# Performance work log

Hardware: AMD Instinct MI355X
Metric: run time of the kernel (lower is better)

## Reference

```python
import jax, jax.numpy as jnp
import numpy as np

B, N, F, H, N_ITERS = 64, 256, 16, 256, 10


def setup_inputs() -> dict:
    key = jax.random.key(0)
    ks = jax.random.split(key, 20)
    s = 0.05
    jets = jax.random.normal(ks[0], (B, N, F), dtype=jnp.float32)
    # row-normalized dense adjacency (D^-1 A style)
    a = jax.random.uniform(ks[1], (B, N, N), dtype=jnp.float32)
    dads = a / jnp.sum(a, axis=-1, keepdims=True)
    p = lambda k, sh: jax.random.normal(k, sh, dtype=jnp.float32) * s
    return {
        'jets': jets, 'dads': dads,
        'W_emb': p(ks[2], (F, H)), 'b_emb': jnp.zeros((H,), jnp.float32),
        'W_msg': p(ks[3], (H, H)), 'b_msg': jnp.zeros((H,), jnp.float32),
        # GRU vertex update: input = concat(message[H], s[F]) -> H
        'Wz': p(ks[4], (H + F, H)), 'Uz': p(ks[5], (H, H)), 'bz': jnp.zeros((H,), jnp.float32),
        'Wr': p(ks[6], (H + F, H)), 'Ur': p(ks[7], (H, H)), 'br': jnp.zeros((H,), jnp.float32),
        'Wh': p(ks[8], (H + F, H)), 'Uh': p(ks[9], (H, H)), 'bh': jnp.zeros((H,), jnp.float32),
        'W_r1': p(ks[10], (H, H)), 'b_r1': jnp.zeros((H,), jnp.float32),
        'W_r2': p(ks[11], (H, H)), 'b_r2': jnp.zeros((H,), jnp.float32),
    }


def reference(jets, dads, W_emb, b_emb, W_msg, b_msg,
              Wz, Uz, bz, Wr, Ur, br, Wh, Uh, bh,
              W_r1, b_r1, W_r2, b_r2):
    # Embedding: [B,N,F] -> [B,N,H]
    h = jnp.tanh(jets @ W_emb + b_emb)
    for _ in range(N_ITERS):
        # Message: linear then adjacency aggregation + tanh
        m = jnp.tanh(jnp.matmul(dads, h @ W_msg + b_msg))  # [B,N,H]
        # GRU-style vertex update; input = concat(message, original features s)
        x = jnp.concatenate([m, jets], axis=-1)            # [B,N,H+F]
        z = jax.nn.sigmoid(x @ Wz + h @ Uz + bz)
        r = jax.nn.sigmoid(x @ Wr + h @ Ur + br)
        h_tilde = jnp.tanh(x @ Wh + (r * h) @ Uh + bh)
        h = (1.0 - z) * h + z * h_tilde
    # Readout: per-node MLP then sum over nodes -> [B,H]
    out = jnp.sum(jnp.tanh(h @ W_r1 + b_r1) @ W_r2 + b_r2, axis=1)
    return out
```

## Files before the change

kernel.cpp:

```cpp
#include <hip/hip_runtime.h>

#define DEVI __device__ __forceinline__

typedef __attribute__((ext_vector_type(4))) float f32x4;
typedef __attribute__((ext_vector_type(8))) short s16x8;
typedef unsigned short u16;
typedef unsigned int u32;

#define WST 288
#define SROW 264
#define AST 264

#define WAITVM(n) __builtin_amdgcn_s_waitcnt(((n)&0xF) | 0x70 | 0xF00 | (((n)>>4)<<14))

DEVI u16 f2bf(float x){
  u32 u = __float_as_uint(x);
  u = (u + 0x7fffu + ((u >> 16) & 1u)) >> 16;
  return (u16)u;
}
DEVI float bf2f(u16 v){ return __uint_as_float(((u32)v) << 16); }

DEVI float fsigm(float x){ return __builtin_amdgcn_rcpf(1.f + __builtin_amdgcn_exp2f(-1.442695041f * x)); }
DEVI float ftanh(float x){ float e = __builtin_amdgcn_exp2f(2.885390082f * x); return 1.f - 2.f * __builtin_amdgcn_rcpf(e + 1.f); }

DEVI s16x8 ld8(const u16* p){ return *(const s16x8*)p; }

DEVI f32x4 ld4bf(const u16* p){
  uint2 v = *(const uint2*)p;
  f32x4 r;
  r[0] = bf2f((u16)(v.x & 0xffff)); r[1] = bf2f((u16)(v.x >> 16));
  r[2] = bf2f((u16)(v.y & 0xffff)); r[3] = bf2f((u16)(v.y >> 16));
  return r;
}

DEVI void st4bf(u16* p, float a, float b, float c, float d){
  uint2 v;
  v.x = (u32)f2bf(a) | ((u32)f2bf(b) << 16);
  v.y = (u32)f2bf(c) | ((u32)f2bf(d) << 16);
  *(uint2*)p = v;
}

#define MFMA(a,b,c) __builtin_amdgcn_mfma_f32_16x16x32_bf16((a),(b),(c),0,0,0)

DEVI void dma2(const u16* lanebase, int rowStrideElems, int c, u16* ldsbase){
#pragma unroll
  for(int q = 0; q < 2; q++){
    const u16* g = lanebase + (size_t)q*16*rowStrideElems + c*32;
    __builtin_amdgcn_global_load_lds((__attribute__((address_space(1))) const void*)g,
                                     (__attribute__((address_space(3))) void*)(ldsbase + q*512),
                                     16, 0, 0);
  }
}
#define AFRAG(buf, t) ld8(&(buf)[(t)*512 + ln*32 + ((qd ^ ((ln>>1)&3))*8)])

__global__ void k_prep(
  const float* __restrict__ jets, const float* __restrict__ dads, const float* __restrict__ W_emb,
  const float* __restrict__ W_msg, const float* __restrict__ Wz, const float* __restrict__ Uz,
  const float* __restrict__ Wr, const float* __restrict__ Ur, const float* __restrict__ Wh,
  const float* __restrict__ Uh, const float* __restrict__ W_r1,
  u16* __restrict__ jp, u16* __restrict__ dadsb, u16* __restrict__ Wet, u16* __restrict__ Wmt,
  u16* __restrict__ Wzt, u16* __restrict__ Uzt, u16* __restrict__ Wrt, u16* __restrict__ Urt,
  u16* __restrict__ Wht, u16* __restrict__ Uht, u16* __restrict__ Wr1t)
{
  int blk = blockIdx.x, tid = threadIdx.x;
  if(blk < 1280){
    int mi = blk >> 8, k = blk & 255, j = tid;
    const float* src; u16* dst;
    switch(mi){
      case 0: src = W_msg; dst = Wmt;  break;
      case 1: src = Uz;    dst = Uzt;  break;
      case 2: src = Ur;    dst = Urt;  break;
      case 3: src = Uh;    dst = Uht;  break;
      default: src = W_r1; dst = Wr1t; break;
    }
    dst[j*256 + k] = f2bf(src[k*256 + j]);
  } else if(blk < 2144){
    int q = blk - 1280; int mi = q / 288; int k = q - mi*288; int j = tid;
    const float* src; u16* dst;
    switch(mi){ case 0: src = Wz; dst = Wzt; break; case 1: src = Wr; dst = Wrt; break; default: src = Wh; dst = Wht; break; }
    dst[j*WST + k] = (k < 272) ? f2bf(src[k*256 + j]) : (u16)0;
  } else if(blk < 2176){
    int idx = (blk - 2144)*256 + tid;
    int j = idx >> 5, k = idx & 31;
    Wet[idx] = (k < 16) ? f2bf(W_emb[k*256 + j]) : (u16)0;
  } else if(blk < 4224){
    int idx = (blk - 2176)*256 + tid;
    int n = idx >> 5, k = idx & 31;
    jp[idx] = (k < 16) ? f2bf(jets[n*16 + k]) : (u16)0;
  } else {
    int idx = (blk - 4224)*256 + tid;
    f32x4 v = *(const f32x4*)(dads + (size_t)idx*4);
    st4bf(dadsb + (size_t)idx*4, v[0], v[1], v[2], v[3]);
  }
}

__global__ __launch_bounds__(256,3) void k_embed(
  u16* __restrict__ h, u16* __restrict__ hmo,
  const u16* __restrict__ jp, const u16* __restrict__ Wet, const float* __restrict__ be,
  const u16* __restrict__ Wmt, const float* __restrict__ bm)
{
  __shared__ u16 hbuf[16*SROW];
  const int tid = threadIdx.x;
  const int wv = tid >> 6, lane = tid & 63, ln = lane & 15, qd = lane >> 4;
  const int n0 = blockIdx.x * 16;
  const int b  = n0 >> 8;
  const int nb = n0 & 255;
  const int nodeA = n0 + ln;

  s16x8 jfr = ld8(jp + (size_t)nodeA*32 + qd*8);
#pragma unroll
  for(int t = 0; t < 4; t++){
    int j0 = (wv*4 + t) * 16;
    f32x4 acc = {0.f,0.f,0.f,0.f};
    s16x8 a = ld8(Wet + (size_t)(j0 + ln)*32 + qd*8);
    acc = MFMA(a, jfr, acc);
    f32x4 bv = *(const f32x4*)(be + j0 + qd*4);
    f32x4 hv;
#pragma unroll
    for(int r = 0; r < 4; r++) hv[r] = ftanh(acc[r] + bv[r]);
    st4bf(h + (size_t)nodeA*256 + j0 + qd*4, hv[0], hv[1], hv[2], hv[3]);
    st4bf(&hbuf[ln*SROW + j0 + qd*4], hv[0], hv[1], hv[2], hv[3]);
  }
  __syncthreads();

  s16x8 af[8];
#pragma unroll
  for(int c = 0; c < 8; c++) af[c] = ld8(&hbuf[ln*SROW + c*32 + qd*8]);
#pragma unroll
  for(int tp = 0; tp < 2; tp++){
    int j0 = (wv*4 + tp*2) * 16, j1 = j0 + 16;
    f32x4 a0 = {0.f,0.f,0.f,0.f}, a1 = {0.f,0.f,0.f,0.f};
#pragma unroll
    for(int c = 0; c < 8; c++){
      a0 = MFMA(af[c], ld8(Wmt + (size_t)(j0 + ln)*256 + c*32 + qd*8), a0);
      a1 = MFMA(af[c], ld8(Wmt + (size_t)(j1 + ln)*256 + c*32 + qd*8), a1);
    }
    float b0 = bm[j0 + ln], b1 = bm[j1 + ln];
    st4bf(hmo + (size_t)(b*256 + j0 + ln)*256 + nb + qd*4, a0[0]+b0, a0[1]+b0, a0[2]+b0, a0[3]+b0);
    st4bf(hmo + (size_t)(b*256 + j1 + ln)*256 + nb + qd*4, a1[0]+b1, a1[1]+b1, a1[2]+b1, a1[3]+b1);
  }
}

__global__ __launch_bounds__(512,1) void k_gru(
  u16* __restrict__ h,
  const u16* __restrict__ hmi, u16* __restrict__ hmo,
  const u16* __restrict__ dadsb, const u16* __restrict__ jp,
  const u16* __restrict__ Wzt, const u16* __restrict__ Wrt, const u16* __restrict__ Wht,
  const u16* __restrict__ Uzt, const u16* __restrict__ Urt, const u16* __restrict__ Uht,
  const u16* __restrict__ Wmt,
  const float* __restrict__ bz, const float* __restrict__ br, const float* __restrict__ bhb,
  const float* __restrict__ bm)
{
  __shared__ u16 smM[64*AST];
  __shared__ u16 smB[64*AST];
  __shared__ __align__(16) u16 stg[8][2][2][1024];
  const int tid = threadIdx.x;
  const int wv = tid >> 6, lane = tid & 63, ln = lane & 15, qd = lane >> 4;
  const int blk   = blockIdx.x;
  const int batch = (blk & 7) * 8 + (blk >> 5);
  const int group = (blk >> 3) & 3;
  const int n0 = batch * 256 + group * 64;
  const int b  = batch;
  const int nb = group * 64;
  const int j0w = wv * 32;

  u16* s0 = &stg[wv][0][0][0];
  u16* s1 = &stg[wv][1][0][0];
  u16* u0 = &stg[wv][0][1][0];
  u16* u1 = &stg[wv][1][1][0];

  const int rw = lane >> 2;
  const int cs = ((lane & 3) ^ ((lane >> 3) & 3)) * 8;

  const u16* laneA = hmi + (size_t)(b*256 + j0w + rw)*256 + cs;
  dma2(laneA, 256, 0, s0);

  s16x8 jB[4];
#pragma unroll
  for(int i = 0; i < 4; i++) jB[i] = ld8(jp + (size_t)(n0 + i*16 + ln)*32 + qd*8);

  {
    f32x4 acc[2][4];
#pragma unroll
    for(int t = 0; t < 2; t++)
#pragma unroll
      for(int i = 0; i < 4; i++) acc[t][i] = (f32x4){0.f,0.f,0.f,0.f};
    s16x8 Bf[4], Bn[4];
#pragma unroll
    for(int i = 0; i < 4; i++) Bf[i] = ld8(dadsb + (size_t)(n0 + i*16 + ln)*256 + qd*8);
#pragma unroll
    for(int c = 0; c < 8; c++){
      u16* cur = (c & 1) ? s1 : s0;
      if(c < 7){
        dma2(laneA, 256, c+1, (c & 1) ? s0 : s1);
#pragma unroll
        for(int i = 0; i < 4; i++) Bn[i] = ld8(dadsb + (size_t)(n0 + i*16 + ln)*256 + (c+1)*32 + qd*8);
        WAITVM(6);
      } else {
        WAITVM(0);
      }
#pragma unroll
      for(int t = 0; t < 2; t++){
        s16x8 A = AFRAG(cur, t);
#pragma unroll
        for(int i = 0; i < 4; i++) acc[t][i] = MFMA(A, Bf[i], acc[t][i]);
      }
      if(c < 7){
#pragma unroll
        for(int i = 0; i < 4; i++) Bf[i] = Bn[i];
      }
    }
#pragma unroll
    for(int t = 0; t < 2; t++)
#pragma unroll
      for(int i = 0; i < 4; i++)
        st4bf(&smM[(i*16 + ln)*AST + j0w + t*16 + qd*4],
              ftanh(acc[t][i][0]), ftanh(acc[t][i][1]), ftanh(acc[t][i][2]), ftanh(acc[t][i][3]));
  }
  const u16* laneWr = Wrt + (size_t)(j0w + rw)*WST + cs;
  const u16* laneUr = Urt + (size_t)(j0w + rw)*256 + cs;
  dma2(laneWr, WST, 0, s0);
  dma2(laneUr, 256, 0, u0);
  __syncthreads();

  {
    f32x4 acc[2][4];
#pragma unroll
    for(int t = 0; t < 2; t++)
#pragma unroll
      for(int i = 0; i < 4; i++) acc[t][i] = (f32x4){0.f,0.f,0.f,0.f};
    s16x8 Aj[2];
#pragma unroll
    for(int t = 0; t < 2; t++) Aj[t] = ld8(Wrt + (size_t)(j0w + t*16 + ln)*WST + 256 + qd*8);
    s16x8 Bh[4], Bn[4];
#pragma unroll
    for(int i = 0; i < 4; i++) Bh[i] = ld8(h + (size_t)(n0 + i*16 + ln)*256 + qd*8);
#pragma unroll
    for(int c = 0; c < 8; c++){
      u16* cw = (c & 1) ? s1 : s0;
      u16* cu = (c & 1) ? u1 : u0;
      if(c < 7){
        dma2(laneWr, WST, c+1, (c & 1) ? s0 : s1);
        dma2(laneUr, 256, c+1, (c & 1) ? u0 : u1);
#pragma unroll
        for(int i = 0; i < 4; i++) Bn[i] = ld8(h + (size_t)(n0 + i*16 + ln)*256 + (c+1)*32 + qd*8);
        WAITVM(8);
      } else {
        WAITVM(0);
      }
      s16x8 Bm[4];
#pragma unroll
      for(int i = 0; i < 4; i++) Bm[i] = ld8(&smM[(i*16 + ln)*AST + c*32 + qd*8]);
#pragma unroll
      for(int t = 0; t < 2; t++){
        s16x8 Aw = AFRAG(cw, t);
#pragma unroll
        for(int i = 0; i < 4; i++) acc[t][i] = MFMA(Aw, Bm[i], acc[t][i]);
      }
#pragma unroll
      for(int t = 0; t < 2; t++){
        s16x8 Au = AFRAG(cu, t);
#pragma unroll
        for(int i = 0; i < 4; i++) acc[t][i] = MFMA(Au, Bh[i], acc[t][i]);
      }
      if(c < 7){
#pragma unroll
        for(int i = 0; i < 4; i++) Bh[i] = Bn[i];
      }
    }
#pragma unroll
    for(int t = 0; t < 2; t++)
#pragma unroll
      for(int i = 0; i < 4; i++) acc[t][i] = MFMA(Aj[t], jB[i], acc[t][i]);
#pragma unroll
    for(int t = 0; t < 2; t++){
      f32x4 bv = *(const f32x4*)(br + j0w + t*16 + qd*4);
#pragma unroll
      for(int i = 0; i < 4; i++){
        f32x4 hv = ld4bf(h + (size_t)(n0 + i*16 + ln)*256 + j0w + t*16 + qd*4);
        st4bf(&smB[(i*16 + ln)*AST + j0w + t*16 + qd*4],
              fsigm(acc[t][i][0]+bv[0])*hv[0], fsigm(acc[t][i][1]+bv[1])*hv[1],
              fsigm(acc[t][i][2]+bv[2])*hv[2], fsigm(acc[t][i][3]+bv[3])*hv[3]);
      }
    }
  }
  const u16* laneWz = Wzt + (size_t)(j0w + rw)*WST + cs;
  const u16* laneUz = Uzt + (size_t)(j0w + rw)*256 + cs;
  dma2(laneWz, WST, 0, s0);
  dma2(laneUz, 256, 0, u0);
  __syncthreads();

  f32x4 zacc[2][4], gacc[2][4];
#pragma unroll
  for(int t = 0; t < 2; t++)
#pragma unroll
    for(int i = 0; i < 4; i++) zacc[t][i] = (f32x4){0.f,0.f,0.f,0.f};
  {
    s16x8 Aj[2];
#pragma unroll
    for(int t = 0; t < 2; t++) Aj[t] = ld8(Wzt + (size_t)(j0w + t*16 + ln)*WST + 256 + qd*8);
    s16x8 Bh[4], Bn[4];
#pragma unroll
    for(int i = 0; i < 4; i++) Bh[i] = ld8(h + (size_t)(n0 + i*16 + ln)*256 + qd*8);
#pragma unroll
    for(int c = 0; c < 8; c++){
      u16* cw = (c & 1) ? s1 : s0;
      u16* cu = (c & 1) ? u1 : u0;
      if(c < 7){
        dma2(laneWz, WST, c+1, (c & 1) ? s0 : s1);
        dma2(laneUz, 256, c+1, (c & 1) ? u0 : u1);
#pragma unroll
        for(int i = 0; i < 4; i++) Bn[i] = ld8(h + (size_t)(n0 + i*16 + ln)*256 + (c+1)*32 + qd*8);
        WAITVM(8);
      } else {
        WAITVM(0);
      }
      s16x8 Bm[4];
#pragma unroll
      for(int i = 0; i < 4; i++) Bm[i] = ld8(&smM[(i*16 + ln)*AST + c*32 + qd*8]);
#pragma unroll
      for(int t = 0; t < 2; t++){
        s16x8 Aw = AFRAG(cw, t);
#pragma unroll
        for(int i = 0; i < 4; i++) zacc[t][i] = MFMA(Aw, Bm[i], zacc[t][i]);
      }
#pragma unroll
      for(int t = 0; t < 2; t++){
        s16x8 Au = AFRAG(cu, t);
#pragma unroll
        for(int i = 0; i < 4; i++) zacc[t][i] = MFMA(Au, Bh[i], zacc[t][i]);
      }
      if(c < 7){
#pragma unroll
        for(int i = 0; i < 4; i++) Bh[i] = Bn[i];
      }
    }
#pragma unroll
    for(int t = 0; t < 2; t++)
#pragma unroll
      for(int i = 0; i < 4; i++) zacc[t][i] = MFMA(Aj[t], jB[i], zacc[t][i]);
  }

  const u16* laneWh = Wht + (size_t)(j0w + rw)*WST + cs;
  const u16* laneUh = Uht + (size_t)(j0w + rw)*256 + cs;
  dma2(laneWh, WST, 0, s0);
  dma2(laneUh, 256, 0, u0);

#pragma unroll
  for(int t = 0; t < 2; t++)
#pragma unroll
    for(int i = 0; i < 4; i++) gacc[t][i] = (f32x4){0.f,0.f,0.f,0.f};
  {
    s16x8 Aj[2];
#pragma unroll
    for(int t = 0; t < 2; t++) Aj[t] = ld8(Wht + (size_t)(j0w + t*16 + ln)*WST + 256 + qd*8);
#pragma unroll
    for(int c = 0; c < 8; c++){
      u16* cw = (c & 1) ? s1 : s0;
      u16* cu = (c & 1) ? u1 : u0;
      if(c < 7){
        dma2(laneWh, WST, c+1, (c & 1) ? s0 : s1);
        dma2(laneUh, 256, c+1, (c & 1) ? u0 : u1);
        WAITVM(4);
      } else {
        WAITVM(0);
      }
      s16x8 Bm[4], Brh[4];
#pragma unroll
      for(int i = 0; i < 4; i++){
        Bm[i]  = ld8(&smM[(i*16 + ln)*AST + c*32 + qd*8]);
        Brh[i] = ld8(&smB[(i*16 + ln)*AST + c*32 + qd*8]);
      }
#pragma unroll
      for(int t = 0; t < 2; t++){
        s16x8 Aw = AFRAG(cw, t);
#pragma unroll
        for(int i = 0; i < 4; i++) gacc[t][i] = MFMA(Aw, Bm[i], gacc[t][i]);
      }
#pragma unroll
      for(int t = 0; t < 2; t++){
        s16x8 Au = AFRAG(cu, t);
#pragma unroll
        for(int i = 0; i < 4; i++) gacc[t][i] = MFMA(Au, Brh[i], gacc[t][i]);
      }
    }
#pragma unroll
    for(int t = 0; t < 2; t++)
#pragma unroll
      for(int i = 0; i < 4; i++) gacc[t][i] = MFMA(Aj[t], jB[i], gacc[t][i]);
  }
  const u16* laneWm = Wmt + (size_t)(j0w + rw)*256 + cs;
  dma2(laneWm, 256, 0, s0);
  __syncthreads();

#pragma unroll
  for(int t = 0; t < 2; t++){
    f32x4 bzv = *(const f32x4*)(bz + j0w + t*16 + qd*4);
    f32x4 bhv = *(const f32x4*)(bhb + j0w + t*16 + qd*4);
#pragma unroll
    for(int i = 0; i < 4; i++){
      f32x4 hv = ld4bf(h + (size_t)(n0 + i*16 + ln)*256 + j0w + t*16 + qd*4);
      f32x4 hn;
#pragma unroll
      for(int r = 0; r < 4; r++){
        float z  = fsigm(zacc[t][i][r] + bzv[r]);
        float th = ftanh(gacc[t][i][r] + bhv[r]);
        hn[r] = hv[r] + z * (th - hv[r]);
      }
      st4bf(h + (size_t)(n0 + i*16 + ln)*256 + j0w + t*16 + qd*4, hn[0], hn[1], hn[2], hn[3]);
      st4bf(&smM[(i*16 + ln)*AST + j0w + t*16 + qd*4], hn[0], hn[1], hn[2], hn[3]);
    }
  }
  __syncthreads();

  {
    f32x4 acc[2][4];
#pragma unroll
    for(int t = 0; t < 2; t++)
#pragma unroll
      for(int i = 0; i < 4; i++) acc[t][i] = (f32x4){0.f,0.f,0.f,0.f};
#pragma unroll
    for(int c = 0; c < 8; c++){
      u16* cur = (c & 1) ? s1 : s0;
      if(c < 7){
        dma2(laneWm, 256, c+1, (c & 1) ? s0 : s1);
        WAITVM(2);
      } else {
        WAITVM(0);
      }
      s16x8 Bf[4];
#pragma unroll
      for(int i = 0; i < 4; i++) Bf[i] = ld8(&smM[(i*16 + ln)*AST + c*32 + qd*8]);
#pragma unroll
      for(int t = 0; t < 2; t++){
        s16x8 A = AFRAG(cur, t);
#pragma unroll
        for(int i = 0; i < 4; i++) acc[t][i] = MFMA(A, Bf[i], acc[t][i]);
      }
    }
#pragma unroll
    for(int t = 0; t < 2; t++){
      f32x4 bmv = *(const f32x4*)(bm + j0w + t*16 + qd*4);
#pragma unroll
      for(int i = 0; i < 4; i++){
#pragma unroll
        for(int r = 0; r < 4; r++){
          hmo[(size_t)(b*256 + j0w + t*16 + qd*4 + r)*256 + nb + i*16 + ln] =
            f2bf(acc[t][i][r] + bmv[r]);
        }
      }
    }
  }
}

__global__ __launch_bounds__(256,3) void k_t(
  const u16* __restrict__ h, u16* __restrict__ t_out,
  const u16* __restrict__ Wr1t, const float* __restrict__ br1)
{
  const int tid = threadIdx.x;
  const int wv = tid >> 6, lane = tid & 63, ln = lane & 15, qd = lane >> 4;
  const int n0 = blockIdx.x * 16;
  const int nodeA = n0 + ln;

  s16x8 hfr[8];
#pragma unroll
  for(int c = 0; c < 8; c++) hfr[c] = ld8(h + (size_t)nodeA*256 + c*32 + qd*8);
#pragma unroll
  for(int tp = 0; tp < 2; tp++){
    int j0 = (wv*4 + tp*2) * 16, j1 = j0 + 16;
    f32x4 a0 = {0.f,0.f,0.f,0.f}, a1 = {0.f,0.f,0.f,0.f};
#pragma unroll
    for(int c = 0; c < 8; c++){
      a0 = MFMA(ld8(Wr1t + (size_t)(j0 + ln)*256 + c*32 + qd*8), hfr[c], a0);
      a1 = MFMA(ld8(Wr1t + (size_t)(j1 + ln)*256 + c*32 + qd*8), hfr[c], a1);
    }
    f32x4 b0 = *(const f32x4*)(br1 + j0 + qd*4);
    f32x4 b1 = *(const f32x4*)(br1 + j1 + qd*4);
    st4bf(t_out + (size_t)nodeA*256 + j0 + qd*4,
          ftanh(a0[0]+b0[0]), ftanh(a0[1]+b0[1]), ftanh(a0[2]+b0[2]), ftanh(a0[3]+b0[3]));
    st4bf(t_out + (size_t)nodeA*256 + j1 + qd*4,
          ftanh(a1[0]+b1[0]), ftanh(a1[1]+b1[1]), ftanh(a1[2]+b1[2]), ftanh(a1[3]+b1[3]));
  }
}

__global__ void k_red(const u16* __restrict__ t, const float* __restrict__ W_r2,
                      const float* __restrict__ b_r2, float* __restrict__ out){
  __shared__ float s[256];
  int b = blockIdx.x, k = threadIdx.x;
  float acc = 0.f;
  for(int n = 0; n < 256; n++) acc += bf2f(t[(size_t)(b*256 + n)*256 + k]);
  s[k] = acc;
  __syncthreads();
  int j = threadIdx.x;
  float o = 256.f * b_r2[j];
  for(int k2 = 0; k2 < 256; k2++) o += s[k2] * W_r2[k2*256 + j];
  out[b*256 + j] = o;
}

extern "C" void kernel_launch(void* const* d_in, const int* in_sizes, int n_in,
                              void* d_out, int out_size, void* d_ws, size_t ws_size,
                              hipStream_t stream)
{
  const float* jets  = (const float*)d_in[0];
  const float* dads  = (const float*)d_in[1];
  const float* W_emb = (const float*)d_in[2];
  const float* b_emb = (const float*)d_in[3];
  const float* W_msg = (const float*)d_in[4];
  const float* b_msg = (const float*)d_in[5];
  const float* Wz    = (const float*)d_in[6];
  const float* Uz    = (const float*)d_in[7];
  const float* bz    = (const float*)d_in[8];
  const float* Wr    = (const float*)d_in[9];
  const float* Ur    = (const float*)d_in[10];
  const float* br    = (const float*)d_in[11];
  const float* Wh    = (const float*)d_in[12];
  const float* Uh    = (const float*)d_in[13];
  const float* bh    = (const float*)d_in[14];
  const float* W_r1  = (const float*)d_in[15];
  const float* b_r1  = (const float*)d_in[16];
  const float* W_r2  = (const float*)d_in[17];
  const float* b_r2  = (const float*)d_in[18];

  char* ws = (char*)d_ws;
  u16* h      = (u16*)(ws);
  u16* hmA    = (u16*)(ws + 8388608);
  u16* hmB    = (u16*)(ws + 16777216);
  u16* dadsb  = (u16*)(ws + 25165824);
  u16* jp     = (u16*)(ws + 33554432);
  u16* Wmt    = (u16*)(ws + 34603008);
  u16* Uzt    = (u16*)(ws + 34734080);
  u16* Urt    = (u16*)(ws + 34865152);
  u16* Uht    = (u16*)(ws + 34996224);
  u16* Wr1t   = (u16*)(ws + 35127296);
  u16* Wzt    = (u16*)(ws + 35258368);
  u16* Wrt    = (u16*)(ws + 35405824);
  u16* Wht    = (u16*)(ws + 35553280);
  u16* Wet    = (u16*)(ws + 35700736);
  float* outp = (float*)d_out;

  k_prep<<<8320, 256, 0, stream>>>(jets, dads, W_emb, W_msg, Wz, Uz, Wr, Ur, Wh, Uh, W_r1,
                                   jp, dadsb, Wet, Wmt, Wzt, Uzt, Wrt, Urt, Wht, Uht, Wr1t);
  k_embed<<<1024, 256, 0, stream>>>(h, hmA, jp, Wet, b_emb, Wmt, b_msg);
  for(int it = 0; it < 10; ++it){
    const u16* hin = (it & 1) ? hmB : hmA;
    u16* hout      = (it & 1) ? hmA : hmB;
    k_gru<<<256, 512, 0, stream>>>(h, hin, hout, dadsb, jp,
                                   Wzt, Wrt, Wht, Uzt, Urt, Uht, Wmt,
                                   bz, br, bh, b_msg);
  }
  k_t<<<1024, 256, 0, stream>>>(h, hmB, Wr1t, b_r1);
  k_red<<<64, 256, 0, stream>>>(hmB, W_r2, b_r2, outp);
}
```

Measured before the change: 598.5 us.

## Fuse r and z gate GEMMs with direct global weight loads and repad LDS

Computes the r and z gate accumulations in one pass over K. A and B fragments are loaded once per chunk and feed both gates, and the r/z weights are read directly from global memory instead of being staged into LDS through the double-buffered DMA pipeline. The LDS activation row stride changes from 264 to 260, and the B fragments are read as two 64-bit loads so the odd stride stays aligned and bank conflicts may drop. The cost is more live accumulator registers, which can lower occupancy, and unpipelined global weight loads whose latency may not be hidden.

```diff
diff --git a/kernel.cpp b/kernel.cpp
--- a/kernel.cpp
+++ b/kernel.cpp
@@ -4,12 +4,13 @@
 
 typedef __attribute__((ext_vector_type(4))) float f32x4;
 typedef __attribute__((ext_vector_type(8))) short s16x8;
+typedef __attribute__((ext_vector_type(4))) short s16x4;
 typedef unsigned short u16;
 typedef unsigned int u32;
 
 #define WST 288
 #define SROW 264
-#define AST 264
+#define AST 260
 
 #define WAITVM(n) __builtin_amdgcn_s_waitcnt(((n)&0xF) | 0x70 | 0xF00 | (((n)>>4)<<14))
 
@@ -24,6 +25,14 @@
 DEVI float ftanh(float x){ float e = __builtin_amdgcn_exp2f(2.885390082f * x); return 1.f - 2.f * __builtin_amdgcn_rcpf(e + 1.f); }
 
 DEVI s16x8 ld8(const u16* p){ return *(const s16x8*)p; }
+DEVI s16x8 ldb64p(const u16* p){
+  s16x4 lo = *(const s16x4*)p;
+  s16x4 hi = *(const s16x4*)(p + 4);
+  s16x8 r;
+  r[0]=lo[0]; r[1]=lo[1]; r[2]=lo[2]; r[3]=lo[3];
+  r[4]=hi[0]; r[5]=hi[1]; r[6]=hi[2]; r[7]=hi[3];
+  return r;
+}
 
 DEVI f32x4 ld4bf(const u16* p){
   uint2 v = *(const uint2*)p;
@@ -217,61 +226,58 @@
         st4bf(&smM[(i*16 + ln)*AST + j0w + t*16 + qd*4],
               ftanh(acc[t][i][0]), ftanh(acc[t][i][1]), ftanh(acc[t][i][2]), ftanh(acc[t][i][3]));
   }
-  const u16* laneWr = Wrt + (size_t)(j0w + rw)*WST + cs;
-  const u16* laneUr = Urt + (size_t)(j0w + rw)*256 + cs;
-  dma2(laneWr, WST, 0, s0);
-  dma2(laneUr, 256, 0, u0);
-  __syncthreads();
-
+  __syncthreads();
+
+  f32x4 racc[2][4], zacc[2][4], gacc[2][4];
+#pragma unroll
+  for(int t = 0; t < 2; t++)
+#pragma unroll
+    for(int i = 0; i < 4; i++){
+      racc[t][i] = (f32x4){0.f,0.f,0.f,0.f};
+      zacc[t][i] = (f32x4){0.f,0.f,0.f,0.f};
+      gacc[t][i] = (f32x4){0.f,0.f,0.f,0.f};
+    }
   {
-    f32x4 acc[2][4];
-#pragma unroll
-    for(int t = 0; t < 2; t++)
-#pragma unroll
-      for(int i = 0; i < 4; i++) acc[t][i] = (f32x4){0.f,0.f,0.f,0.f};
-    s16x8 Aj[2];
-#pragma unroll
-    for(int t = 0; t < 2; t++) Aj[t] = ld8(Wrt + (size_t)(j0w + t*16 + ln)*WST + 256 + qd*8);
-    s16x8 Bh[4], Bn[4];
-#pragma unroll
-    for(int i = 0; i < 4; i++) Bh[i] = ld8(h + (size_t)(n0 + i*16 + ln)*256 + qd*8);
-#pragma unroll
-    for(int c = 0; c < 8; c++){
-      u16* cw = (c & 1) ? s1 : s0;
-      u16* cu = (c & 1) ? u1 : u0;
-      if(c < 7){
-        dma2(laneWr, WST, c+1, (c & 1) ? s0 : s1);
-        dma2(laneUr, 256, c+1, (c & 1) ? u0 : u1);
-#pragma unroll
-        for(int i = 0; i < 4; i++) Bn[i] = ld8(h + (size_t)(n0 + i*16 + ln)*256 + (c+1)*32 + qd*8);
-        WAITVM(8);
-      } else {
-        WAITVM(0);
-      }
-      s16x8 Bm[4];
-#pragma unroll
-      for(int i = 0; i < 4; i++) Bm[i] = ld8(&smM[(i*16 + ln)*AST + c*32 + qd*8]);
+#pragma unroll
+    for(int c = 0; c < 8; c++){
+      s16x8 Awr[2], Awz[2], Aur[2], Auz[2];
 #pragma unroll
       for(int t = 0; t < 2; t++){
-        s16x8 Aw = AFRAG(cw, t);
-#pragma unroll
-        for(int i = 0; i < 4; i++) acc[t][i] = MFMA(Aw, Bm[i], acc[t][i]);
-      }
-#pragma unroll
-      for(int t = 0; t < 2; t++){
-        s16x8 Au = AFRAG(cu, t);
-#pragma unroll
-        for(int i = 0; i < 4; i++) acc[t][i] = MFMA(Au, Bh[i], acc[t][i]);
-      }
-      if(c < 7){
-#pragma unroll
-        for(int i = 0; i < 4; i++) Bh[i] = Bn[i];
-      }
-    }
-#pragma unroll
-    for(int t = 0; t < 2; t++)
-#pragma unroll
-      for(int i = 0; i < 4; i++) acc[t][i] = MFMA(Aj[t], jB[i], acc[t][i]);
+        Awr[t] = ld8(Wrt + (size_t)(j0w + t*16 + ln)*WST + c*32 + qd*8);
+        Awz[t] = ld8(Wzt + (size_t)(j0w + t*16 + ln)*WST + c*32 + qd*8);
+        Aur[t] = ld8(Urt + (size_t)(j0w + t*16 + ln)*256 + c*32 + qd*8);
+        Auz[t] = ld8(Uzt + (size_t)(j0w + t*16 + ln)*256 + c*32 + qd*8);
+      }
+      s16x8 Bh[4], Bm[4];
+#pragma unroll
+      for(int i = 0; i < 4; i++) Bh[i] = ld8(h + (size_t)(n0 + i*16 + ln)*256 + c*32 + qd*8);
+#pragma unroll
+      for(int i = 0; i < 4; i++) Bm[i] = ldb64p(&smM[(i*16 + ln)*AST + c*32 + qd*8]);
+#pragma unroll
+      for(int t = 0; t < 2; t++)
+#pragma unroll
+        for(int i = 0; i < 4; i++){
+          racc[t][i] = MFMA(Awr[t], Bm[i], racc[t][i]);
+          zacc[t][i] = MFMA(Awz[t], Bm[i], zacc[t][i]);
+        }
+#pragma unroll
+      for(int t = 0; t < 2; t++)
+#pragma unroll
+        for(int i = 0; i < 4; i++){
+          racc[t][i] = MFMA(Aur[t], Bh[i], racc[t][i]);
+          zacc[t][i] = MFMA(Auz[t], Bh[i], zacc[t][i]);
+        }
+    }
+#pragma unroll
+    for(int t = 0; t < 2; t++){
+      s16x8 Ajr = ld8(Wrt + (size_t)(j0w + t*16 + ln)*WST + 256 + qd*8);
+      s16x8 Ajz = ld8(Wzt + (size_t)(j0w + t*16 + ln)*WST + 256 + qd*8);
+#pragma unroll
+      for(int i = 0; i < 4; i++){
+        racc[t][i] = MFMA(Ajr, jB[i], racc[t][i]);
+        zacc[t][i] = MFMA(Ajz, jB[i], zacc[t][i]);
+      }
+    }
 #pragma unroll
     for(int t = 0; t < 2; t++){
       f32x4 bv = *(const f32x4*)(br + j0w + t*16 + qd*4);
@@ -279,81 +285,18 @@
       for(int i = 0; i < 4; i++){
         f32x4 hv = ld4bf(h + (size_t)(n0 + i*16 + ln)*256 + j0w + t*16 + qd*4);
         st4bf(&smB[(i*16 + ln)*AST + j0w + t*16 + qd*4],
-              fsigm(acc[t][i][0]+bv[0])*hv[0], fsigm(acc[t][i][1]+bv[1])*hv[1],
-              fsigm(acc[t][i][2]+bv[2])*hv[2], fsigm(acc[t][i][3]+bv[3])*hv[3]);
-      }
-    }
-  }
-  const u16* laneWz = Wzt + (size_t)(j0w + rw)*WST + cs;
-  const u16* laneUz = Uzt + (size_t)(j0w + rw)*256 + cs;
-  dma2(laneWz, WST, 0, s0);
-  dma2(laneUz, 256, 0, u0);
-  __syncthreads();
-
-  f32x4 zacc[2][4], gacc[2][4];
-#pragma unroll
-  for(int t = 0; t < 2; t++)
-#pragma unroll
-    for(int i = 0; i < 4; i++) zacc[t][i] = (f32x4){0.f,0.f,0.f,0.f};
-  {
-    s16x8 Aj[2];
-#pragma unroll
-    for(int t = 0; t < 2; t++) Aj[t] = ld8(Wzt + (size_t)(j0w + t*16 + ln)*WST + 256 + qd*8);
-    s16x8 Bh[4], Bn[4];
-#pragma unroll
-    for(int i = 0; i < 4; i++) Bh[i] = ld8(h + (size_t)(n0 + i*16 + ln)*256 + qd*8);
-#pragma unroll
-    for(int c = 0; c < 8; c++){
-      u16* cw = (c & 1) ? s1 : s0;
-      u16* cu = (c & 1) ? u1 : u0;
-      if(c < 7){
-        dma2(laneWz, WST, c+1, (c & 1) ? s0 : s1);
-        dma2(laneUz, 256, c+1, (c & 1) ? u0 : u1);
-#pragma unroll
-        for(int i = 0; i < 4; i++) Bn[i] = ld8(h + (size_t)(n0 + i*16 + ln)*256 + (c+1)*32 + qd*8);
-        WAITVM(8);
-      } else {
-        WAITVM(0);
-      }
-      s16x8 Bm[4];
-#pragma unroll
-      for(int i = 0; i < 4; i++) Bm[i] = ld8(&smM[(i*16 + ln)*AST + c*32 + qd*8]);
-#pragma unroll
-      for(int t = 0; t < 2; t++){
-        s16x8 Aw = AFRAG(cw, t);
-#pragma unroll
-        for(int i = 0; i < 4; i++) zacc[t][i] = MFMA(Aw, Bm[i], zacc[t][i]);
-      }
-#pragma unroll
-      for(int t = 0; t < 2; t++){
-        s16x8 Au = AFRAG(cu, t);
-#pragma unroll
-        for(int i = 0; i < 4; i++) zacc[t][i] = MFMA(Au, Bh[i], zacc[t][i]);
-      }
-      if(c < 7){
-#pragma unroll
-        for(int i = 0; i < 4; i++) Bh[i] = Bn[i];
-      }
-    }
-#pragma unroll
-    for(int t = 0; t < 2; t++)
-#pragma unroll
-      for(int i = 0; i < 4; i++) zacc[t][i] = MFMA(Aj[t], jB[i], zacc[t][i]);
-  }
-
+              fsigm(racc[t][i][0]+bv[0])*hv[0], fsigm(racc[t][i][1]+bv[1])*hv[1],
+              fsigm(racc[t][i][2]+bv[2])*hv[2], fsigm(racc[t][i][3]+bv[3])*hv[3]);
+      }
+    }
+  }
   const u16* laneWh = Wht + (size_t)(j0w + rw)*WST + cs;
   const u16* laneUh = Uht + (size_t)(j0w + rw)*256 + cs;
   dma2(laneWh, WST, 0, s0);
   dma2(laneUh, 256, 0, u0);
-
-#pragma unroll
-  for(int t = 0; t < 2; t++)
-#pragma unroll
-    for(int i = 0; i < 4; i++) gacc[t][i] = (f32x4){0.f,0.f,0.f,0.f};
+  __syncthreads();
+
   {
-    s16x8 Aj[2];
-#pragma unroll
-    for(int t = 0; t < 2; t++) Aj[t] = ld8(Wht + (size_t)(j0w + t*16 + ln)*WST + 256 + qd*8);
 #pragma unroll
     for(int c = 0; c < 8; c++){
       u16* cw = (c & 1) ? s1 : s0;
@@ -368,8 +311,8 @@
       s16x8 Bm[4], Brh[4];
 #pragma unroll
       for(int i = 0; i < 4; i++){
-        Bm[i]  = ld8(&smM[(i*16 + ln)*AST + c*32 + qd*8]);
-        Brh[i] = ld8(&smB[(i*16 + ln)*AST + c*32 + qd*8]);
+        Bm[i]  = ldb64p(&smM[(i*16 + ln)*AST + c*32 + qd*8]);
+        Brh[i] = ldb64p(&smB[(i*16 + ln)*AST + c*32 + qd*8]);
       }
 #pragma unroll
       for(int t = 0; t < 2; t++){
@@ -385,12 +328,12 @@
       }
     }
 #pragma unroll
-    for(int t = 0; t < 2; t++)
-#pragma unroll
-      for(int i = 0; i < 4; i++) gacc[t][i] = MFMA(Aj[t], jB[i], gacc[t][i]);
-  }
-  const u16* laneWm = Wmt + (size_t)(j0w + rw)*256 + cs;
-  dma2(laneWm, 256, 0, s0);
+    for(int t = 0; t < 2; t++){
+      s16x8 Ajh = ld8(Wht + (size_t)(j0w + t*16 + ln)*WST + 256 + qd*8);
+#pragma unroll
+      for(int i = 0; i < 4; i++) gacc[t][i] = MFMA(Ajh, jB[i], gacc[t][i]);
+    }
+  }
   __syncthreads();
 
 #pragma unroll
@@ -411,6 +354,8 @@
       st4bf(&smM[(i*16 + ln)*AST + j0w + t*16 + qd*4], hn[0], hn[1], hn[2], hn[3]);
     }
   }
+  const u16* laneWm = Wmt + (size_t)(j0w + rw)*256 + cs;
+  dma2(laneWm, 256, 0, s0);
   __syncthreads();
 
   {
@@ -430,7 +375,7 @@
       }
       s16x8 Bf[4];
 #pragma unroll
-      for(int i = 0; i < 4; i++) Bf[i] = ld8(&smM[(i*16 + ln)*AST + c*32 + qd*8]);
+      for(int i = 0; i < 4; i++) Bf[i] = ldb64p(&smM[(i*16 + ln)*AST + c*32 + qd*8]);
 #pragma unroll
       for(int t = 0; t < 2; t++){
         s16x8 A = AFRAG(cur, t);
```

After: 631.0 us. 1.05x slower.

## Use 4 waves with 64-column tiles per wave in GRU kernel

Applied to the files above, without the earlier changes.

The GRU kernel now runs with 256 threads (4 waves) instead of 512, and each wave computes 64 output columns instead of 32. This doubles the accumulator tiles per wave so each B fragment loaded from LDS or global feeds twice as many MFMAs, and the weight staging DMA moves four row-groups per call. The LDS row pitch for smM/smB changes to 260 elements, read with paired 64-bit loads, which is aimed at LDS bank conflicts. The Wm prefetch is moved after the h update. In exchange, register pressure rises a lot (zacc and gacc are now 32 f32x4), and fewer waves per CU remain to hide latency.

```diff
diff --git a/kernel.cpp b/kernel.cpp
--- a/kernel.cpp
+++ b/kernel.cpp
@@ -4,12 +4,13 @@
 
 typedef __attribute__((ext_vector_type(4))) float f32x4;
 typedef __attribute__((ext_vector_type(8))) short s16x8;
+typedef __attribute__((ext_vector_type(4))) short s16x4;
 typedef unsigned short u16;
 typedef unsigned int u32;
 
 #define WST 288
 #define SROW 264
-#define AST 264
+#define AST 260
 
 #define WAITVM(n) __builtin_amdgcn_s_waitcnt(((n)&0xF) | 0x70 | 0xF00 | (((n)>>4)<<14))
 
@@ -24,6 +25,14 @@
 DEVI float ftanh(float x){ float e = __builtin_amdgcn_exp2f(2.885390082f * x); return 1.f - 2.f * __builtin_amdgcn_rcpf(e + 1.f); }
 
 DEVI s16x8 ld8(const u16* p){ return *(const s16x8*)p; }
+DEVI s16x8 ldb64p(const u16* p){
+  s16x4 lo = *(const s16x4*)p;
+  s16x4 hi = *(const s16x4*)(p + 4);
+  s16x8 r;
+  r[0]=lo[0]; r[1]=lo[1]; r[2]=lo[2]; r[3]=lo[3];
+  r[4]=hi[0]; r[5]=hi[1]; r[6]=hi[2]; r[7]=hi[3];
+  return r;
+}
 
 DEVI f32x4 ld4bf(const u16* p){
   uint2 v = *(const uint2*)p;
@@ -42,9 +51,9 @@
 
 #define MFMA(a,b,c) __builtin_amdgcn_mfma_f32_16x16x32_bf16((a),(b),(c),0,0,0)
 
-DEVI void dma2(const u16* lanebase, int rowStrideElems, int c, u16* ldsbase){
-#pragma unroll
-  for(int q = 0; q < 2; q++){
+DEVI void dma4(const u16* lanebase, int rowStrideElems, int c, u16* ldsbase){
+#pragma unroll
+  for(int q = 0; q < 4; q++){
     const u16* g = lanebase + (size_t)q*16*rowStrideElems + c*32;
     __builtin_amdgcn_global_load_lds((__attribute__((address_space(1))) const void*)g,
                                      (__attribute__((address_space(3))) void*)(ldsbase + q*512),
@@ -141,7 +150,7 @@
   }
 }
 
-__global__ __launch_bounds__(512,1) void k_gru(
+__global__ __launch_bounds__(256,1) void k_gru(
   u16* __restrict__ h,
   const u16* __restrict__ hmi, u16* __restrict__ hmo,
   const u16* __restrict__ dadsb, const u16* __restrict__ jp,
@@ -153,7 +162,7 @@
 {
   __shared__ u16 smM[64*AST];
   __shared__ u16 smB[64*AST];
-  __shared__ __align__(16) u16 stg[8][2][2][1024];
+  __shared__ __align__(16) u16 stg[4][2][2][2048];
   const int tid = threadIdx.x;
   const int wv = tid >> 6, lane = tid & 63, ln = lane & 15, qd = lane >> 4;
   const int blk   = blockIdx.x;
@@ -162,7 +171,7 @@
   const int n0 = batch * 256 + group * 64;
   const int b  = batch;
   const int nb = group * 64;
-  const int j0w = wv * 32;
+  const int j0w = wv * 64;
 
   u16* s0 = &stg[wv][0][0][0];
   u16* s1 = &stg[wv][1][0][0];
@@ -173,16 +182,16 @@
   const int cs = ((lane & 3) ^ ((lane >> 3) & 3)) * 8;
 
   const u16* laneA = hmi + (size_t)(b*256 + j0w + rw)*256 + cs;
-  dma2(laneA, 256, 0, s0);
+  dma4(laneA, 256, 0, s0);
 
   s16x8 jB[4];
 #pragma unroll
   for(int i = 0; i < 4; i++) jB[i] = ld8(jp + (size_t)(n0 + i*16 + ln)*32 + qd*8);
 
   {
-    f32x4 acc[2][4];
-#pragma unroll
-    for(int t = 0; t < 2; t++)
+    f32x4 acc[4][4];
+#pragma unroll
+    for(int t = 0; t < 4; t++)
 #pragma unroll
       for(int i = 0; i < 4; i++) acc[t][i] = (f32x4){0.f,0.f,0.f,0.f};
     s16x8 Bf[4], Bn[4];
@@ -192,15 +201,15 @@
     for(int c = 0; c < 8; c++){
       u16* cur = (c & 1) ? s1 : s0;
       if(c < 7){
-        dma2(laneA, 256, c+1, (c & 1) ? s0 : s1);
+        dma4(laneA, 256, c+1, (c & 1) ? s0 : s1);
 #pragma unroll
         for(int i = 0; i < 4; i++) Bn[i] = ld8(dadsb + (size_t)(n0 + i*16 + ln)*256 + (c+1)*32 + qd*8);
-        WAITVM(6);
+        WAITVM(8);
       } else {
         WAITVM(0);
       }
 #pragma unroll
-      for(int t = 0; t < 2; t++){
+      for(int t = 0; t < 4; t++){
         s16x8 A = AFRAG(cur, t);
 #pragma unroll
         for(int i = 0; i < 4; i++) acc[t][i] = MFMA(A, Bf[i], acc[t][i]);
@@ -211,7 +220,7 @@
       }
     }
 #pragma unroll
-    for(int t = 0; t < 2; t++)
+    for(int t = 0; t < 4; t++)
 #pragma unroll
       for(int i = 0; i < 4; i++)
         st4bf(&smM[(i*16 + ln)*AST + j0w + t*16 + qd*4],
@@ -219,19 +228,19 @@
   }
   const u16* laneWr = Wrt + (size_t)(j0w + rw)*WST + cs;
   const u16* laneUr = Urt + (size_t)(j0w + rw)*256 + cs;
-  dma2(laneWr, WST, 0, s0);
-  dma2(laneUr, 256, 0, u0);
+  dma4(laneWr, WST, 0, s0);
+  dma4(laneUr, 256, 0, u0);
   __syncthreads();
 
   {
-    f32x4 acc[2][4];
-#pragma unroll
-    for(int t = 0; t < 2; t++)
+    f32x4 acc[4][4];
+#pragma unroll
+    for(int t = 0; t < 4; t++)
 #pragma unroll
       for(int i = 0; i < 4; i++) acc[t][i] = (f32x4){0.f,0.f,0.f,0.f};
-    s16x8 Aj[2];
-#pragma unroll
-    for(int t = 0; t < 2; t++) Aj[t] = ld8(Wrt + (size_t)(j0w + t*16 + ln)*WST + 256 + qd*8);
+    s16x8 Aj[4];
+#pragma unroll
+    for(int t = 0; t < 4; t++) Aj[t] = ld8(Wrt + (size_t)(j0w + t*16 + ln)*WST + 256 + qd*8);
     s16x8 Bh[4], Bn[4];
 #pragma unroll
     for(int i = 0; i < 4; i++) Bh[i] = ld8(h + (size_t)(n0 + i*16 + ln)*256 + qd*8);
@@ -240,25 +249,25 @@
       u16* cw = (c & 1) ? s1 : s0;
       u16* cu = (c & 1) ? u1 : u0;
       if(c < 7){
-        dma2(laneWr, WST, c+1, (c & 1) ? s0 : s1);
-        dma2(laneUr, 256, c+1, (c & 1) ? u0 : u1);
+        dma4(laneWr, WST, c+1, (c & 1) ? s0 : s1);
+        dma4(laneUr, 256, c+1, (c & 1) ? u0 : u1);
 #pragma unroll
         for(int i = 0; i < 4; i++) Bn[i] = ld8(h + (size_t)(n0 + i*16 + ln)*256 + (c+1)*32 + qd*8);
-        WAITVM(8);
+        WAITVM(12);
       } else {
         WAITVM(0);
       }
       s16x8 Bm[4];
 #pragma unroll
-      for(int i = 0; i < 4; i++) Bm[i] = ld8(&smM[(i*16 + ln)*AST + c*32 + qd*8]);
-#pragma unroll
-      for(int t = 0; t < 2; t++){
+      for(int i = 0; i < 4; i++) Bm[i] = ldb64p(&smM[(i*16 + ln)*AST + c*32 + qd*8]);
+#pragma unroll
+      for(int t = 0; t < 4; t++){
         s16x8 Aw = AFRAG(cw, t);
 #pragma unroll
         for(int i = 0; i < 4; i++) acc[t][i] = MFMA(Aw, Bm[i], acc[t][i]);
       }
 #pragma unroll
-      for(int t = 0; t < 2; t++){
+      for(int t = 0; t < 4; t++){
         s16x8 Au = AFRAG(cu, t);
 #pragma unroll
         for(int i = 0; i < 4; i++) acc[t][i] = MFMA(Au, Bh[i], acc[t][i]);
@@ -269,11 +278,11 @@
       }
     }
 #pragma unroll
-    for(int t = 0; t < 2; t++)
+    for(int t = 0; t < 4; t++)
 #pragma unroll
       for(int i = 0; i < 4; i++) acc[t][i] = MFMA(Aj[t], jB[i], acc[t][i]);
 #pragma unroll
-    for(int t = 0; t < 2; t++){
+    for(int t = 0; t < 4; t++){
       f32x4 bv = *(const f32x4*)(br + j0w + t*16 + qd*4);
 #pragma unroll
       for(int i = 0; i < 4; i++){
@@ -286,19 +295,19 @@
   }
   const u16* laneWz = Wzt + (size_t)(j0w + rw)*WST + cs;
   const u16* laneUz = Uzt + (size_t)(j0w + rw)*256 + cs;
-  dma2(laneWz, WST, 0, s0);
-  dma2(laneUz, 256, 0, u0);
+  dma4(laneWz, WST, 0, s0);
+  dma4(laneUz, 256, 0, u0);
   __syncthreads();
 
-  f32x4 zacc[2][4], gacc[2][4];
-#pragma unroll
-  for(int t = 0; t < 2; t++)
+  f32x4 zacc[4][4], gacc[4][4];
+#pragma unroll
+  for(int t = 0; t < 4; t++)
 #pragma unroll
     for(int i = 0; i < 4; i++) zacc[t][i] = (f32x4){0.f,0.f,0.f,0.f};
   {
-    s16x8 Aj[2];
-#pragma unroll
-    for(int t = 0; t < 2; t++) Aj[t] = ld8(Wzt + (size_t)(j0w + t*16 + ln)*WST + 256 + qd*8);
+    s16x8 Aj[4];
+#pragma unroll
+    for(int t = 0; t < 4; t++) Aj[t] = ld8(Wzt + (size_t)(j0w + t*16 + ln)*WST + 256 + qd*8);
     s16x8 Bh[4], Bn[4];
 #pragma unroll
     for(int i = 0; i < 4; i++) Bh[i] = ld8(h + (size_t)(n0 + i*16 + ln)*256 + qd*8);
@@ -307,94 +316,92 @@
       u16* cw = (c & 1) ? s1 : s0;
       u16* cu = (c & 1) ? u1 : u0;
       if(c < 7){
-        dma2(laneWz, WST, c+1, (c & 1) ? s0 : s1);
-        dma2(laneUz, 256, c+1, (c & 1) ? u0 : u1);
+        dma4(laneWz, WST, c+1, (c & 1) ? s0 : s1);
+        dma4(laneUz, 256, c+1, (c & 1) ? u0 : u1);
 #pragma unroll
         for(int i = 0; i < 4; i++) Bn[i] = ld8(h + (size_t)(n0 + i*16 + ln)*256 + (c+1)*32 + qd*8);
+        WAITVM(12);
+      } else {
+        WAITVM(0);
+      }
+      s16x8 Bm[4];
+#pragma unroll
+      for(int i = 0; i < 4; i++) Bm[i] = ldb64p(&smM[(i*16 + ln)*AST + c*32 + qd*8]);
+#pragma unroll
+      for(int t = 0; t < 4; t++){
+        s16x8 Aw = AFRAG(cw, t);
+#pragma unroll
+        for(int i = 0; i < 4; i++) zacc[t][i] = MFMA(Aw, Bm[i], zacc[t][i]);
+      }
+#pragma unroll
+      for(int t = 0; t < 4; t++){
+        s16x8 Au = AFRAG(cu, t);
+#pragma unroll
+        for(int i = 0; i < 4; i++) zacc[t][i] = MFMA(Au, Bh[i], zacc[t][i]);
+      }
+      if(c < 7){
+#pragma unroll
+        for(int i = 0; i < 4; i++) Bh[i] = Bn[i];
+      }
+    }
+#pragma unroll
+    for(int t = 0; t < 4; t++)
+#pragma unroll
+      for(int i = 0; i < 4; i++) zacc[t][i] = MFMA(Aj[t], jB[i], zacc[t][i]);
+  }
+
+  const u16* laneWh = Wht + (size_t)(j0w + rw)*WST + cs;
+  const u16* laneUh = Uht + (size_t)(j0w + rw)*256 + cs;
+  dma4(laneWh, WST, 0, s0);
+  dma4(laneUh, 256, 0, u0);
+
+#pragma unroll
+  for(int t = 0; t < 4; t++)
+#pragma unroll
+    for(int i = 0; i < 4; i++) gacc[t][i] = (f32x4){0.f,0.f,0.f,0.f};
+  {
+    s16x8 Aj[4];
+#pragma unroll
+    for(int t = 0; t < 4; t++) Aj[t] = ld8(Wht + (size_t)(j0w + t*16 + ln)*WST + 256 + qd*8);
+#pragma unroll
+    for(int c = 0; c < 8; c++){
+      u16* cw = (c & 1) ? s1 : s0;
+      u16* cu = (c & 1) ? u1 : u0;
+      if(c < 7){
+        dma4(laneWh, WST, c+1, (c & 1) ? s0 : s1);
+        dma4(laneUh, 256, c+1, (c & 1) ? u0 : u1);
         WAITVM(8);
       } else {
         WAITVM(0);
       }
-      s16x8 Bm[4];
-#pragma unroll
-      for(int i = 0; i < 4; i++) Bm[i] = ld8(&smM[(i*16 + ln)*AST + c*32 + qd*8]);
-#pragma unroll
-      for(int t = 0; t < 2; t++){
+      s16x8 Bm[4], Brh[4];
+#pragma unroll
+      for(int i = 0; i < 4; i++){
+        Bm[i]  = ldb64p(&smM[(i*16 + ln)*AST + c*32 + qd*8]);
+        Brh[i] = ldb64p(&smB[(i*16 + ln)*AST + c*32 + qd*8]);
+      }
+#pragma unroll
+      for(int t = 0; t < 4; t++){
         s16x8 Aw = AFRAG(cw, t);
 #pragma unroll
-        for(int i = 0; i < 4; i++) zacc[t][i] = MFMA(Aw, Bm[i], zacc[t][i]);
-      }
-#pragma unroll
-      for(int t = 0; t < 2; t++){
+        for(int i = 0; i < 4; i++) gacc[t][i] = MFMA(Aw, Bm[i], gacc[t][i]);
+      }
+#pragma unroll
+      for(int t = 0; t < 4; t++){
         s16x8 Au = AFRAG(cu, t);
 #pragma unroll
-        for(int i = 0; i < 4; i++) zacc[t][i] = MFMA(Au, Bh[i], zacc[t][i]);
-      }
-      if(c < 7){
-#pragma unroll
-        for(int i = 0; i < 4; i++) Bh[i] = Bn[i];
-      }
-    }
-#pragma unroll
-    for(int t = 0; t < 2; t++)
-#pragma unroll
-      for(int i = 0; i < 4; i++) zacc[t][i] = MFMA(Aj[t], jB[i], zacc[t][i]);
-  }
-
-  const u16* laneWh = Wht + (size_t)(j0w + rw)*WST + cs;
-  const u16* laneUh = Uht + (size_t)(j0w + rw)*256 + cs;
-  dma2(laneWh, WST, 0, s0);
-  dma2(laneUh, 256, 0, u0);
-
-#pragma unroll
-  for(int t = 0; t < 2; t++)
-#pragma unroll
-    for(int i = 0; i < 4; i++) gacc[t][i] = (f32x4){0.f,0.f,0.f,0.f};
-  {
-    s16x8 Aj[2];
-#pragma unroll
-    for(int t = 0; t < 2; t++) Aj[t] = ld8(Wht + (size_t)(j0w + t*16 + ln)*WST + 256 + qd*8);
-#pragma unroll
-    for(int c = 0; c < 8; c++){
-      u16* cw = (c & 1) ? s1 : s0;
-      u16* cu = (c & 1) ? u1 : u0;
-      if(c < 7){
-        dma2(laneWh, WST, c+1, (c & 1) ? s0 : s1);
-        dma2(laneUh, 256, c+1, (c & 1) ? u0 : u1);
-        WAITVM(4);
-      } else {
-        WAITVM(0);
-      }
-      s16x8 Bm[4], Brh[4];
-#pragma unroll
-      for(int i = 0; i < 4; i++){
-        Bm[i]  = ld8(&smM[(i*16 + ln)*AST + c*32 + qd*8]);
-        Brh[i] = ld8(&smB[(i*16 + ln)*AST + c*32 + qd*8]);
-      }
-#pragma unroll
-      for(int t = 0; t < 2; t++){
-        s16x8 Aw = AFRAG(cw, t);
-#pragma unroll
-        for(int i = 0; i < 4; i++) gacc[t][i] = MFMA(Aw, Bm[i], gacc[t][i]);
-      }
-#pragma unroll
-      for(int t = 0; t < 2; t++){
-        s16x8 Au = AFRAG(cu, t);
-#pragma unroll
         for(int i = 0; i < 4; i++) gacc[t][i] = MFMA(Au, Brh[i], gacc[t][i]);
       }
     }
 #pragma unroll
-    for(int t = 0; t < 2; t++)
+    for(int t = 0; t < 4; t++)
 #pragma unroll
       for(int i = 0; i < 4; i++) gacc[t][i] = MFMA(Aj[t], jB[i], gacc[t][i]);
   }
-  const u16* laneWm = Wmt + (size_t)(j0w + rw)*256 + cs;
-  dma2(laneWm, 256, 0, s0);
   __syncthreads();
 
 #pragma unroll
-  for(int t = 0; t < 2; t++){
+  for(int t = 0; t < 4; t++){
     f32x4 bzv = *(const f32x4*)(bz + j0w + t*16 + qd*4);
     f32x4 bhv = *(const f32x4*)(bhb + j0w + t*16 + qd*4);
 #pragma unroll
@@ -411,35 +418,37 @@
       st4bf(&smM[(i*16 + ln)*AST + j0w + t*16 + qd*4], hn[0], hn[1], hn[2], hn[3]);
     }
   }
+  const u16* laneWm = Wmt + (size_t)(j0w + rw)*256 + cs;
+  dma4(laneWm, 256, 0, s0);
   __syncthreads();
 
   {
-    f32x4 acc[2][4];
-#pragma unroll
-    for(int t = 0; t < 2; t++)
+    f32x4 acc[4][4];
+#pragma unroll
+    for(int t = 0; t < 4; t++)
 #pragma unroll
       for(int i = 0; i < 4; i++) acc[t][i] = (f32x4){0.f,0.f,0.f,0.f};
 #pragma unroll
     for(int c = 0; c < 8; c++){
       u16* cur = (c & 1) ? s1 : s0;
       if(c < 7){
-        dma2(laneWm, 256, c+1, (c & 1) ? s0 : s1);
-        WAITVM(2);
+        dma4(laneWm, 256, c+1, (c & 1) ? s0 : s1);
+        WAITVM(4);
       } else {
         WAITVM(0);
       }
       s16x8 Bf[4];
 #pragma unroll
-      for(int i = 0; i < 4; i++) Bf[i] = ld8(&smM[(i*16 + ln)*AST + c*32 + qd*8]);
-#pragma unroll
-      for(int t = 0; t < 2; t++){
+      for(int i = 0; i < 4; i++) Bf[i] = ldb64p(&smM[(i*16 + ln)*AST + c*32 + qd*8]);
+#pragma unroll
+      for(int t = 0; t < 4; t++){
         s16x8 A = AFRAG(cur, t);
 #pragma unroll
         for(int i = 0; i < 4; i++) acc[t][i] = MFMA(A, Bf[i], acc[t][i]);
       }
     }
 #pragma unroll
-    for(int t = 0; t < 2; t++){
+    for(int t = 0; t < 4; t++){
       f32x4 bmv = *(const f32x4*)(bm + j0w + t*16 + qd*4);
 #pragma unroll
       for(int i = 0; i < 4; i++){
@@ -544,7 +553,7 @@
   for(int it = 0; it < 10; ++it){
     const u16* hin = (it & 1) ? hmB : hmA;
     u16* hout      = (it & 1) ? hmA : hmB;
-    k_gru<<<256, 512, 0, stream>>>(h, hin, hout, dadsb, jp,
+    k_gru<<<256, 256, 0, stream>>>(h, hin, hout, dadsb, jp,
                                    Wzt, Wrt, Wht, Uzt, Urt, Uht, Wmt,
                                    bz, br, bh, b_msg);
   }
```

New measurement: 558.9 us. 6.6% less time.
